# Optimization experiments

Measured on AMD Instinct MI355X. Metric: run time of the kernel, lower is better.

The kernel has to match this reference:

```python
import jax, jax.numpy as jnp
import numpy as np

IN_CH = 128
NUM_GROUPS = 32
EPS = 1e-5


def group_norm(x, weight, bias):
    b, c, h, w = x.shape
    g = NUM_GROUPS
    xg = x.reshape(b, g, c // g, h, w)
    mean = xg.mean(axis=(2, 3, 4), keepdims=True)
    var = xg.var(axis=(2, 3, 4), keepdims=True)
    xg = (xg - mean) * jax.lax.rsqrt(var + EPS)
    x = xg.reshape(b, c, h, w)
    return x * weight[None, :, None, None] + bias[None, :, None, None]


def conv1x1(x, w, b):
    # x: (b,c,h,w), w: (out,in), b: (out,)
    return jnp.einsum('oc,bchw->bohw', w, x) + b[None, :, None, None]


def setup_inputs() -> dict:
    key = jax.random.key(0)
    ks = jax.random.split(key, 6)
    b, c, h, w = 8, IN_CH, 64, 64
    scale = 1.0 / np.sqrt(c)  # xavier-ish scale for 1x1 convs
    return {
        'x': jax.random.normal(ks[0], (b, c, h, w), dtype=jnp.float32),
        'gn_weight': jnp.ones((c,), dtype=jnp.float32),
        'gn_bias': jnp.zeros((c,), dtype=jnp.float32),
        'wq': jax.random.normal(ks[1], (c, c), dtype=jnp.float32) * scale,
        'bq': jnp.zeros((c,), dtype=jnp.float32),
        'wk': jax.random.normal(ks[2], (c, c), dtype=jnp.float32) * scale,
        'bk': jnp.zeros((c,), dtype=jnp.float32),
        'wv': jax.random.normal(ks[3], (c, c), dtype=jnp.float32) * scale,
        'bv': jnp.zeros((c,), dtype=jnp.float32),
        'wo': jax.random.normal(ks[4], (c, c), dtype=jnp.float32) * scale,
        'bo': jnp.zeros((c,), dtype=jnp.float32),
        'gamma': jnp.ones((1,), dtype=jnp.float32),
    }


def reference(x, gn_weight, gn_bias, wq, bq, wk, bk, wv, bv, wo, bo, gamma):
    b, c, h, w = x.shape
    x_dash = group_norm(x, gn_weight, gn_bias)
    q = conv1x1(x_dash, wq, bq).reshape(b, c, h * w)  # (b,c,n)
    k = conv1x1(x_dash, wk, bk).reshape(b, c, h * w)
    v = conv1x1(x_dash, wv, bv).reshape(b, c, h * w)
    # attn[b,i,j] = sum_c q[b,c,i] k[b,c,j] / sqrt(c)
    attn = jnp.einsum('bci,bcj->bij', q, k) / jnp.sqrt(jnp.float32(c))
    attn = jax.nn.softmax(attn, axis=-1)
    # out[b,c,i] = sum_j v[b,c,j] attn[b,i,j]
    out = jnp.einsum('bcj,bij->bci', v, attn).reshape(b, c, h, w)
    out = conv1x1(out, wo, bo)
    return x + gamma[0] * out
```

## Files before the change

### kernel.cpp

```cpp
#include <hip/hip_runtime.h>

typedef unsigned short u16;
typedef unsigned int u32;
typedef __bf16 bf16_t;
typedef bf16_t bf16x8 __attribute__((ext_vector_type(8)));
typedef float f32x4 __attribute__((ext_vector_type(4)));
typedef u32 u32x4 __attribute__((ext_vector_type(4)));
typedef u32 u32x2 __attribute__((ext_vector_type(2)));

#define BATCH 8
#define CH 128
#define NSP 4096
#define LOG2E 1.44269504088896f

static __device__ __forceinline__ u16 f2bf(float f) {
  u32 u = __builtin_bit_cast(u32, f);
  u32 r = u + 0x7FFFu + ((u >> 16) & 1u);
  return (u16)(r >> 16);
}

static __device__ __forceinline__ bf16x8 ld_bf8(const u16* p) {
  return __builtin_bit_cast(bf16x8, *(const u32x4*)p);
}

static __device__ __forceinline__ f32x4 mfma16(bf16x8 a, bf16x8 b, f32x4 c) {
  return __builtin_amdgcn_mfma_f32_16x16x32_bf16(a, b, c, 0, 0, 0);
}

static __device__ __forceinline__ u32 cvt_pk(float lo, float hi) {
  u32 r;
  asm("v_cvt_pk_bf16_f32 %0, %1, %2" : "=v"(r) : "v"(lo), "v"(hi));
  return r;
}

static __device__ __forceinline__ float fast_exp2(float x) {
#if __has_builtin(__builtin_amdgcn_exp2f)
  return __builtin_amdgcn_exp2f(x);
#else
  return exp2f(x);
#endif
}

__global__ __launch_bounds__(256) void gn_stats_kernel(const float* __restrict__ x,
                                                       float* __restrict__ stats,
                                                       const float* __restrict__ wq,
                                                       const float* __restrict__ wk,
                                                       const float* __restrict__ wv,
                                                       const float* __restrict__ wo,
                                                       u16* __restrict__ wbf) {
  int bg = blockIdx.x;
  {
    int widx = bg * 256 + threadIdx.x;
    int m = widx >> 14, r = widx & 16383;
    const float* s = (m == 0) ? wq : (m == 1) ? wk : (m == 2) ? wv : wo;
    wbf[widx] = f2bf(s[r]);
  }
  const float4* p = (const float4*)(x + (size_t)bg * 16384);
  float s = 0.f, ss = 0.f;
  for (int i = threadIdx.x; i < 4096; i += 256) {
    float4 v = p[i];
    s += v.x + v.y + v.z + v.w;
    ss += v.x * v.x + v.y * v.y + v.z * v.z + v.w * v.w;
  }
  for (int off = 32; off; off >>= 1) {
    s += __shfl_xor(s, off);
    ss += __shfl_xor(ss, off);
  }
  __shared__ float rs[4], rss[4];
  int wave = threadIdx.x >> 6;
  if ((threadIdx.x & 63) == 0) { rs[wave] = s; rss[wave] = ss; }
  __syncthreads();
  if (threadIdx.x == 0) {
    s = rs[0] + rs[1] + rs[2] + rs[3];
    ss = rss[0] + rss[1] + rss[2] + rss[3];
    float mean = s * (1.f / 16384.f);
    float var = ss * (1.f / 16384.f) - mean * mean;
    stats[2 * bg] = mean;
    stats[2 * bg + 1] = rsqrtf(var + 1e-5f);
  }
}

__global__ __launch_bounds__(256) void qkv_kernel(const float* __restrict__ x,
                                                  const float* __restrict__ stats,
                                                  const float* __restrict__ gnw,
                                                  const float* __restrict__ gnb,
                                                  const u16* __restrict__ wqb,
                                                  const u16* __restrict__ wkb,
                                                  const u16* __restrict__ wvb,
                                                  const float* __restrict__ bq,
                                                  const float* __restrict__ bk,
                                                  const float* __restrict__ bv,
                                                  u16* __restrict__ q, u16* __restrict__ k,
                                                  u16* __restrict__ v) {
  __shared__ float tile[64][132];
  __shared__ float sc[128], sh[128];
  int b = blockIdx.y;
  int n0 = blockIdx.x * 64;
  int t = threadIdx.x;
  if (t < 128) {
    float mean = stats[2 * (b * 32 + (t >> 2))];
    float rstd = stats[2 * (b * 32 + (t >> 2)) + 1];
    float w = gnw[t];
    sc[t] = rstd * w;
    sh[t] = gnb[t] - mean * rstd * w;
  }
  __syncthreads();
  const float4* xb4 = (const float4*)(x + (size_t)b * CH * NSP);
#pragma unroll
  for (int i = 0; i < 8; ++i) {
    int idx = t + i * 256;
    int c = idx >> 4, j4 = idx & 15;
    float4 vv = xb4[(size_t)c * (NSP / 4) + (n0 >> 2) + j4];
    float s_ = sc[c], h_ = sh[c];
    tile[j4 * 4 + 0][c] = vv.x * s_ + h_;
    tile[j4 * 4 + 1][c] = vv.y * s_ + h_;
    tile[j4 * 4 + 2][c] = vv.z * s_ + h_;
    tile[j4 * 4 + 3][c] = vv.w * s_ + h_;
  }
  __syncthreads();

  int wave = t >> 6, lane = t & 63;
  int lr = lane & 15, lg = lane >> 4;
  int n_base = n0 + wave * 16;
  int row = wave * 16 + lr;

  bf16x8 xfr[4];
#pragma unroll
  for (int kk = 0; kk < 4; ++kk) {
    const float* p = &tile[row][kk * 32 + lg * 8];
    f32x4 lo = *(const f32x4*)p;
    f32x4 hi = *(const f32x4*)(p + 4);
    u32x4 xw = {cvt_pk(lo[0], lo[1]), cvt_pk(lo[2], lo[3]),
                cvt_pk(hi[0], hi[1]), cvt_pk(hi[2], hi[3])};
    xfr[kk] = __builtin_bit_cast(bf16x8, xw);
  }

  f32x4 accq[8] = {}, acck[8] = {}, accv[8] = {};
#pragma unroll
  for (int kk = 0; kk < 4; ++kk) {
    int coff = kk * 32 + lg * 8;
    bf16x8 xa = xfr[kk];
#pragma unroll
    for (int ot = 0; ot < 8; ++ot) {
      int woff = (ot * 16 + lr) * CH + coff;
      bf16x8 wqf = ld_bf8(wqb + woff);
      bf16x8 wkf = ld_bf8(wkb + woff);
      bf16x8 wvf = ld_bf8(wvb + woff);
      accq[ot] = mfma16(xa, wqf, accq[ot]);
      acck[ot] = mfma16(xa, wkf, acck[ot]);
      accv[ot] = mfma16(wvf, xa, accv[ot]);
    }
  }
  const float qscale = 0.08838834764831845f * LOG2E;
#pragma unroll
  for (int ot = 0; ot < 8; ++ot) {
    int o_col = ot * 16 + lr;
    float bqv = bq[o_col], bkv = bk[o_col];
#pragma unroll
    for (int r = 0; r < 4; ++r) {
      int nrow = n_base + lg * 4 + r;
      size_t off = ((size_t)b * NSP + nrow) * CH + o_col;
      q[off] = f2bf((accq[ot][r] + bqv) * qscale);
      k[off] = f2bf(acck[ot][r] + bkv);
    }
    int n_col = n_base + lr;
#pragma unroll
    for (int r = 0; r < 4; ++r) {
      int o_row = ot * 16 + lg * 4 + r;
      v[((size_t)b * CH + o_row) * NSP + n_col] = f2bf(accv[ot][r] + bv[o_row]);
    }
  }
}

#define KSTRIDE 136
#define VSTRIDE 72
__global__ __launch_bounds__(256, 2) void attn_kernel(const u16* __restrict__ q,
                                                      const u16* __restrict__ k,
                                                      const u16* __restrict__ v,
                                                      u16* __restrict__ part0,
                                                      u16* __restrict__ part1,
                                                      float* __restrict__ lbuf) {
  __shared__ __align__(16) u16 kbuf[2][64 * KSTRIDE];
  __shared__ __align__(16) u16 vbuf[2][128 * VSTRIDE];
  int id = blockIdx.x;
  int b = id & 7;
  int qblk = (id >> 3) & 31;
  int split = id >> 8;
  int wave = threadIdx.x >> 6, lane = threadIdx.x & 63;
  int lr = lane & 15, lg = lane >> 4;
  int i_base = qblk * 128 + wave * 32;
  int t0 = split * 32, t1 = t0 + 32;

  const u16* kg = k + (size_t)b * NSP * CH;
  const u16* vg = v + (size_t)b * CH * NSP;

  bf16x8 qa[2][4];
#pragma unroll
  for (int qt = 0; qt < 2; ++qt) {
    const u16* qrow = q + ((size_t)b * NSP + i_base + qt * 16 + lr) * CH;
#pragma unroll
    for (int kk = 0; kk < 4; ++kk) qa[qt][kk] = ld_bf8(qrow + kk * 32 + lg * 8);
  }

  int kgo[4], klo[4];
#pragma unroll
  for (int m = 0; m < 4; ++m) {
    int kr = wave * 16 + m * 4 + (lane >> 4);
    kgo[m] = kr * CH + (lane & 15) * 8;
    klo[m] = kr * KSTRIDE + (lane & 15) * 8;
  }
  int vgo[4][2], vlo[4];
  {
    int f = lane & 7;
    int p = ((lane >> 2) & 1) * 8 + (lane & 3);
#pragma unroll
    for (int w = 0; w < 4; ++w) {
      int c = wave * 32 + w * 8 + (lane >> 3);
      vgo[w][0] = c * NSP + p * 4;
      vgo[w][1] = c * NSP + (p + 4) * 4;
      vlo[w] = c * VSTRIDE + f * 8;
    }
  }

  u32x4 kstg[4];
  u32x2 vstg[4][2];
  auto KLOAD = [&](int t) {
    const u16* kt = kg + (size_t)t * (64 * CH);
#pragma unroll
    for (int m = 0; m < 4; ++m) kstg[m] = *(const u32x4*)(kt + kgo[m]);
  };
  auto VLOAD = [&](int t) {
    const u16* vt = vg + t * 64;
#pragma unroll
    for (int w = 0; w < 4; ++w) {
      vstg[w][0] = *(const u32x2*)(vt + vgo[w][0]);
      vstg[w][1] = *(const u32x2*)(vt + vgo[w][1]);
    }
  };
  auto KVWRITE = [&](int bi) {
    u16* kb2 = kbuf[bi];
    u16* vb2 = vbuf[bi];
#pragma unroll
    for (int m = 0; m < 4; ++m) *(u32x4*)(kb2 + klo[m]) = kstg[m];
#pragma unroll
    for (int w = 0; w < 4; ++w) {
      u32x4 d = {vstg[w][0][0], vstg[w][0][1], vstg[w][1][0], vstg[w][1][1]};
      *(u32x4*)(vb2 + vlo[w]) = d;
    }
  };

  KLOAD(t0);
  VLOAD(t0);
  asm volatile("s_waitcnt vmcnt(0)" ::: "memory");
  KVWRITE(0);
  KLOAD(t0 + 1);
  VLOAD(t0 + 1);
  asm volatile("s_waitcnt lgkmcnt(0)" ::: "memory");
  __builtin_amdgcn_s_barrier();
  __builtin_amdgcn_sched_barrier(0);

  f32x4 oacc[2][8] = {};
  float lsum[2] = {0.f, 0.f};

  for (int t = t0; t < t1; ++t) {
    int cur = (t - t0) & 1;
    const u16* kb = kbuf[cur];
    const u16* vb = vbuf[cur];

    f32x4 s[2][4] = {};
    __builtin_amdgcn_s_setprio(1);
#pragma unroll
    for (int kk = 0; kk < 4; ++kk) {
#pragma unroll
      for (int jt = 0; jt < 4; ++jt) {
        int row = jt * 16 + lr;
        bf16x8 kf = ld_bf8(kb + row * KSTRIDE + (kk * 4 + lg) * 8);
        s[0][jt] = mfma16(kf, qa[0][kk], s[0][jt]);
        s[1][jt] = mfma16(kf, qa[1][kk], s[1][jt]);
      }
    }
    __builtin_amdgcn_s_setprio(0);

    u32x4 paw[2][2];
#pragma unroll
    for (int qt = 0; qt < 2; ++qt) {
      float sum = 0.f;
#pragma unroll
      for (int jt = 0; jt < 4; ++jt)
#pragma unroll
        for (int r = 0; r < 4; ++r) {
          float pv = fast_exp2(s[qt][jt][r]);
          s[qt][jt][r] = pv;
          sum += pv;
        }
      lsum[qt] += sum;
#pragma unroll
      for (int kk2 = 0; kk2 < 2; ++kk2) {
        paw[qt][kk2][0] = cvt_pk(s[qt][2 * kk2][0], s[qt][2 * kk2][1]);
        paw[qt][kk2][1] = cvt_pk(s[qt][2 * kk2][2], s[qt][2 * kk2][3]);
        paw[qt][kk2][2] = cvt_pk(s[qt][2 * kk2 + 1][0], s[qt][2 * kk2 + 1][1]);
        paw[qt][kk2][3] = cvt_pk(s[qt][2 * kk2 + 1][2], s[qt][2 * kk2 + 1][3]);
      }
    }

    __builtin_amdgcn_s_setprio(1);
#pragma unroll
    for (int kk2 = 0; kk2 < 2; ++kk2) {
      bf16x8 pa0 = __builtin_bit_cast(bf16x8, paw[0][kk2]);
      bf16x8 pa1 = __builtin_bit_cast(bf16x8, paw[1][kk2]);
#pragma unroll
      for (int ct = 0; ct < 8; ++ct) {
        int c = ct * 16 + lr;
        bf16x8 vf = ld_bf8(vb + c * VSTRIDE + (kk2 * 4 + lg) * 8);
        oacc[0][ct] = mfma16(pa0, vf, oacc[0][ct]);
        oacc[1][ct] = mfma16(pa1, vf, oacc[1][ct]);
      }
    }
    __builtin_amdgcn_s_setprio(0);

    if (t + 1 < t1) {
      asm volatile("s_waitcnt vmcnt(0)" ::: "memory");
      KVWRITE(cur ^ 1);
      if (t + 2 < t1) {
        KLOAD(t + 2);
        VLOAD(t + 2);
      }
      asm volatile("s_waitcnt lgkmcnt(0)" ::: "memory");
      __builtin_amdgcn_s_barrier();
      __builtin_amdgcn_sched_barrier(0);
    }
  }

  u16* pdst = (split == 0) ? part0 : part1;
  float* ldst = lbuf + (size_t)split * (BATCH * NSP) + (size_t)b * NSP;
#pragma unroll
  for (int qt = 0; qt < 2; ++qt) {
    lsum[qt] += __shfl_xor(lsum[qt], 16);
    lsum[qt] += __shfl_xor(lsum[qt], 32);
    if (lg == 0) ldst[i_base + qt * 16 + lr] = lsum[qt];
#pragma unroll
    for (int r = 0; r < 4; ++r) {
      int i = i_base + qt * 16 + lg * 4 + r;
      u16* row = pdst + ((size_t)b * NSP + i) * CH;
#pragma unroll
      for (int ct = 0; ct < 8; ++ct) row[ct * 16 + lr] = f2bf(oacc[qt][ct][r]);
    }
  }
}

__global__ __launch_bounds__(256) void proj_kernel(const u16* __restrict__ p0,
                                                   const u16* __restrict__ p1,
                                                   const float* __restrict__ lbuf,
                                                   const u16* __restrict__ wob,
                                                   const float* __restrict__ bo,
                                                   const float* __restrict__ gamma,
                                                   const float* __restrict__ x,
                                                   float* __restrict__ out) {
  int b = blockIdx.y;
  int wave = threadIdx.x >> 6, lane = threadIdx.x & 63;
  int lr = lane & 15, lg = lane >> 4;
  int n_base = blockIdx.x * 64 + wave * 16;
  int nrow = n_base + lr;
  float linv = 1.f / (lbuf[(size_t)b * NSP + nrow] +
                      lbuf[(size_t)BATCH * NSP + (size_t)b * NSP + nrow]);
  const u16* r0 = p0 + ((size_t)b * NSP + nrow) * CH;
  const u16* r1 = p1 + ((size_t)b * NSP + nrow) * CH;
  f32x4 acc[8] = {};
#pragma unroll
  for (int kk = 0; kk < 4; ++kk) {
    int coff = kk * 32 + lg * 8;
    bf16x8 a = ld_bf8(r0 + coff);
    bf16x8 bb = ld_bf8(r1 + coff);
    u32 w0 = cvt_pk(((float)a[0] + (float)bb[0]) * linv, ((float)a[1] + (float)bb[1]) * linv);
    u32 w1 = cvt_pk(((float)a[2] + (float)bb[2]) * linv, ((float)a[3] + (float)bb[3]) * linv);
    u32 w2 = cvt_pk(((float)a[4] + (float)bb[4]) * linv, ((float)a[5] + (float)bb[5]) * linv);
    u32 w3 = cvt_pk(((float)a[6] + (float)bb[6]) * linv, ((float)a[7] + (float)bb[7]) * linv);
    u32x4 wv = {w0, w1, w2, w3};
    bf16x8 ofrag = __builtin_bit_cast(bf16x8, wv);
#pragma unroll
    for (int ot = 0; ot < 8; ++ot) {
      bf16x8 wf = ld_bf8(wob + (ot * 16 + lr) * CH + coff);
      acc[ot] = mfma16(wf, ofrag, acc[ot]);
    }
  }
  float g = gamma[0];
  int n_col = n_base + lr;
#pragma unroll
  for (int ot = 0; ot < 8; ++ot) {
#pragma unroll
    for (int r = 0; r < 4; ++r) {
      int o_row = ot * 16 + lg * 4 + r;
      size_t off = ((size_t)b * CH + o_row) * NSP + n_col;
      out[off] = x[off] + g * (acc[ot][r] + bo[o_row]);
    }
  }
}

extern "C" void kernel_launch(void* const* d_in, const int* in_sizes, int n_in,
                              void* d_out, int out_size, void* d_ws, size_t ws_size,
                              hipStream_t stream) {
  const float* x = (const float*)d_in[0];
  const float* gnw = (const float*)d_in[1];
  const float* gnb = (const float*)d_in[2];
  const float* wq = (const float*)d_in[3];
  const float* bq = (const float*)d_in[4];
  const float* wk = (const float*)d_in[5];
  const float* bk = (const float*)d_in[6];
  const float* wv = (const float*)d_in[7];
  const float* bv = (const float*)d_in[8];
  const float* wo = (const float*)d_in[9];
  const float* bo = (const float*)d_in[10];
  const float* gamma = (const float*)d_in[11];
  float* out = (float*)d_out;

  const size_t BUF = (size_t)BATCH * NSP * CH * sizeof(u16);
  char* ws = (char*)d_ws;
  u16* wbf = (u16*)ws;
  float* stats = (float*)(ws + 131072);
  u16* xd = (u16*)(ws + 262144);
  u16* qb = (u16*)(ws + 262144 + BUF);
  u16* kb = (u16*)(ws + 262144 + 2 * BUF);
  u16* vb = (u16*)(ws + 262144 + 3 * BUF);
  float* lbuf = (float*)(ws + 262144 + 4 * BUF);
  const size_t need = 262144 + 4 * BUF + 262144;
  if (ws_size < need) return;
  u16* part1 = (ws_size >= need + BUF) ? (u16*)(ws + need) : qb;

  gn_stats_kernel<<<256, 256, 0, stream>>>(x, stats, wq, wk, wv, wo, wbf);
  qkv_kernel<<<dim3(64, 8), 256, 0, stream>>>(x, stats, gnw, gnb, wbf, wbf + 16384,
                                              wbf + 32768, bq, bk, bv, qb, kb, vb);
  attn_kernel<<<512, 256, 0, stream>>>(qb, kb, vb, xd, part1, lbuf);
  proj_kernel<<<dim3(64, 8), 256, 0, stream>>>(xd, part1, lbuf, wbf + 49152, bo, gamma,
                                               x, out);
}
```

Baseline: 135.3 us.

## Stage K/V via direct global-to-LDS loads with swizzled layout and 3-way split

Replaces register-staged K/V tile copies in the attention kernel with global_load_lds direct transfers, using an XOR-swizzled layout written by the QKV kernel instead of padded LDS strides. V becomes single-buffered to cut LDS use, which allows 3 blocks per CU, and the key range is split three ways across 768 blocks. A separate combine kernel normalises the three partials before projection, reusing the output and K buffers as scratch. This trades an extra kernel launch and more partial-buffer traffic for better occupancy and less LDS staging overhead.

Result: slower. 141.7 us (+4.8%).

```diff
diff --git a/kernel.cpp b/kernel.cpp
--- a/kernel.cpp
+++ b/kernel.cpp
@@ -6,7 +6,6 @@
 typedef bf16_t bf16x8 __attribute__((ext_vector_type(8)));
 typedef float f32x4 __attribute__((ext_vector_type(4)));
 typedef u32 u32x4 __attribute__((ext_vector_type(4)));
-typedef u32 u32x2 __attribute__((ext_vector_type(2)));
 
 #define BATCH 8
 #define CH 128
@@ -39,6 +38,11 @@
 #else
   return exp2f(x);
 #endif
+}
+
+static __device__ __forceinline__ void gl2lds16(const u16* g, u16* l) {
+  __builtin_amdgcn_global_load_lds((const __attribute__((address_space(1))) void*)g,
+                                   (__attribute__((address_space(3))) void*)l, 16, 0, 0);
 }
 
 __global__ __launch_bounds__(256) void gn_stats_kernel(const float* __restrict__ x,
@@ -152,6 +156,9 @@
     }
   }
   const float qscale = 0.08838834764831845f * LOG2E;
+  int jj = wave * 16 + lr;
+  int frv = (jj >> 5) * 4 + ((jj & 15) >> 2);
+  int ev = (lr & 3) + ((wave & 1) << 2);
 #pragma unroll
   for (int ot = 0; ot < 8; ++ot) {
     int o_col = ot * 16 + lr;
@@ -159,29 +166,29 @@
 #pragma unroll
     for (int r = 0; r < 4; ++r) {
       int nrow = n_base + lg * 4 + r;
-      size_t off = ((size_t)b * NSP + nrow) * CH + o_col;
-      q[off] = f2bf((accq[ot][r] + bqv) * qscale);
-      k[off] = f2bf(acck[ot][r] + bkv);
-    }
-    int n_col = n_base + lr;
+      q[((size_t)b * NSP + nrow) * CH + o_col] = f2bf((accq[ot][r] + bqv) * qscale);
+      int cperm = ((((o_col >> 3) ^ (nrow & 7)) << 3)) | (o_col & 7);
+      k[((size_t)b * NSP + nrow) * CH + cperm] = f2bf(acck[ot][r] + bkv);
+    }
 #pragma unroll
     for (int r = 0; r < 4; ++r) {
-      int o_row = ot * 16 + lg * 4 + r;
-      v[((size_t)b * CH + o_row) * NSP + n_col] = f2bf(accv[ot][r] + bv[o_row]);
-    }
-  }
-}
-
-#define KSTRIDE 136
-#define VSTRIDE 72
-__global__ __launch_bounds__(256, 2) void attn_kernel(const u16* __restrict__ q,
+      int c = ot * 16 + lg * 4 + r;
+      int slot = frv ^ (c & 7);
+      v[((size_t)(b * CH + c)) * NSP + blockIdx.x * 64 + slot * 8 + ev] =
+          f2bf(accv[ot][r] + bv[c]);
+    }
+  }
+}
+
+__global__ __launch_bounds__(256, 3) void attn_kernel(const u16* __restrict__ q,
                                                       const u16* __restrict__ k,
                                                       const u16* __restrict__ v,
                                                       u16* __restrict__ part0,
                                                       u16* __restrict__ part1,
+                                                      u16* __restrict__ part2,
                                                       float* __restrict__ lbuf) {
-  __shared__ __align__(16) u16 kbuf[2][64 * KSTRIDE];
-  __shared__ __align__(16) u16 vbuf[2][128 * VSTRIDE];
+  __shared__ __align__(16) u16 kbuf[2][64 * 128];
+  __shared__ __align__(16) u16 vbuf[128 * 64];
   int id = blockIdx.x;
   int b = id & 7;
   int qblk = (id >> 3) & 31;
@@ -189,7 +196,8 @@
   int wave = threadIdx.x >> 6, lane = threadIdx.x & 63;
   int lr = lane & 15, lg = lane >> 4;
   int i_base = qblk * 128 + wave * 32;
-  int t0 = split * 32, t1 = t0 + 32;
+  int t0 = (split * 64) / 3;
+  int t1 = ((split + 1) * 64) / 3;
 
   const u16* kg = k + (size_t)b * NSP * CH;
   const u16* vg = v + (size_t)b * CH * NSP;
@@ -201,63 +209,24 @@
 #pragma unroll
     for (int kk = 0; kk < 4; ++kk) qa[qt][kk] = ld_bf8(qrow + kk * 32 + lg * 8);
   }
-
-  int kgo[4], klo[4];
-#pragma unroll
-  for (int m = 0; m < 4; ++m) {
-    int kr = wave * 16 + m * 4 + (lane >> 4);
-    kgo[m] = kr * CH + (lane & 15) * 8;
-    klo[m] = kr * KSTRIDE + (lane & 15) * 8;
-  }
-  int vgo[4][2], vlo[4];
-  {
-    int f = lane & 7;
-    int p = ((lane >> 2) & 1) * 8 + (lane & 3);
-#pragma unroll
-    for (int w = 0; w < 4; ++w) {
-      int c = wave * 32 + w * 8 + (lane >> 3);
-      vgo[w][0] = c * NSP + p * 4;
-      vgo[w][1] = c * NSP + (p + 4) * 4;
-      vlo[w] = c * VSTRIDE + f * 8;
-    }
-  }
-
-  u32x4 kstg[4];
-  u32x2 vstg[4][2];
-  auto KLOAD = [&](int t) {
-    const u16* kt = kg + (size_t)t * (64 * CH);
-#pragma unroll
-    for (int m = 0; m < 4; ++m) kstg[m] = *(const u32x4*)(kt + kgo[m]);
+  asm volatile("s_waitcnt vmcnt(0)" ::: "memory");
+
+  auto STAGEK = [&](int t, int bi) {
+    const u16* src = kg + ((size_t)(t * 64 + wave * 16)) * CH + lane * 8;
+    u16* dst = &kbuf[bi][wave * 16 * 128];
+#pragma unroll
+    for (int g = 0; g < 4; ++g) gl2lds16(src + g * 512, dst + g * 512);
   };
-  auto VLOAD = [&](int t) {
-    const u16* vt = vg + t * 64;
-#pragma unroll
-    for (int w = 0; w < 4; ++w) {
-      vstg[w][0] = *(const u32x2*)(vt + vgo[w][0]);
-      vstg[w][1] = *(const u32x2*)(vt + vgo[w][1]);
-    }
+  int vco = wave * 32 + (lane >> 3);
+  auto STAGEV = [&](int t) {
+    const u16* src = vg + t * 64 + (lane & 7) * 8;
+    u16* dst = &vbuf[wave * 32 * 64];
+#pragma unroll
+    for (int g = 0; g < 4; ++g) gl2lds16(src + (size_t)(vco + g * 8) * NSP, dst + g * 512);
   };
-  auto KVWRITE = [&](int bi) {
-    u16* kb2 = kbuf[bi];
-    u16* vb2 = vbuf[bi];
-#pragma unroll
-    for (int m = 0; m < 4; ++m) *(u32x4*)(kb2 + klo[m]) = kstg[m];
-#pragma unroll
-    for (int w = 0; w < 4; ++w) {
-      u32x4 d = {vstg[w][0][0], vstg[w][0][1], vstg[w][1][0], vstg[w][1][1]};
-      *(u32x4*)(vb2 + vlo[w]) = d;
-    }
-  };
-
-  KLOAD(t0);
-  VLOAD(t0);
-  asm volatile("s_waitcnt vmcnt(0)" ::: "memory");
-  KVWRITE(0);
-  KLOAD(t0 + 1);
-  VLOAD(t0 + 1);
-  asm volatile("s_waitcnt lgkmcnt(0)" ::: "memory");
-  __builtin_amdgcn_s_barrier();
-  __builtin_amdgcn_sched_barrier(0);
+
+  STAGEK(t0, 0);
+  STAGEV(t0);
 
   f32x4 oacc[2][8] = {};
   float lsum[2] = {0.f, 0.f};
@@ -265,7 +234,14 @@
   for (int t = t0; t < t1; ++t) {
     int cur = (t - t0) & 1;
     const u16* kb = kbuf[cur];
-    const u16* vb = vbuf[cur];
+    if (t + 1 < t1) {
+      STAGEK(t + 1, cur ^ 1);
+      asm volatile("s_waitcnt vmcnt(4)" ::: "memory");
+    } else {
+      asm volatile("s_waitcnt vmcnt(0)" ::: "memory");
+    }
+    __builtin_amdgcn_s_barrier();
+    __builtin_amdgcn_sched_barrier(0);
 
     f32x4 s[2][4] = {};
     __builtin_amdgcn_s_setprio(1);
@@ -274,7 +250,7 @@
 #pragma unroll
       for (int jt = 0; jt < 4; ++jt) {
         int row = jt * 16 + lr;
-        bf16x8 kf = ld_bf8(kb + row * KSTRIDE + (kk * 4 + lg) * 8);
+        bf16x8 kf = ld_bf8(kb + row * 128 + ((((kk << 2) + lg) ^ (row & 7)) << 3));
         s[0][jt] = mfma16(kf, qa[0][kk], s[0][jt]);
         s[1][jt] = mfma16(kf, qa[1][kk], s[1][jt]);
       }
@@ -311,27 +287,18 @@
 #pragma unroll
       for (int ct = 0; ct < 8; ++ct) {
         int c = ct * 16 + lr;
-        bf16x8 vf = ld_bf8(vb + c * VSTRIDE + (kk2 * 4 + lg) * 8);
+        bf16x8 vf = ld_bf8(vbuf + c * 64 + ((((kk2 << 2) + lg) ^ (c & 7)) << 3));
         oacc[0][ct] = mfma16(pa0, vf, oacc[0][ct]);
         oacc[1][ct] = mfma16(pa1, vf, oacc[1][ct]);
       }
     }
     __builtin_amdgcn_s_setprio(0);
 
-    if (t + 1 < t1) {
-      asm volatile("s_waitcnt vmcnt(0)" ::: "memory");
-      KVWRITE(cur ^ 1);
-      if (t + 2 < t1) {
-        KLOAD(t + 2);
-        VLOAD(t + 2);
-      }
-      asm volatile("s_waitcnt lgkmcnt(0)" ::: "memory");
-      __builtin_amdgcn_s_barrier();
-      __builtin_amdgcn_sched_barrier(0);
-    }
-  }
-
-  u16* pdst = (split == 0) ? part0 : part1;
+    __builtin_amdgcn_s_barrier();
+    if (t + 1 < t1) STAGEV(t + 1);
+  }
+
+  u16* pdst = (split == 0) ? part0 : (split == 1) ? part1 : part2;
   float* ldst = lbuf + (size_t)split * (BATCH * NSP) + (size_t)b * NSP;
 #pragma unroll
   for (int qt = 0; qt < 2; ++qt) {
@@ -348,9 +315,27 @@
   }
 }
 
-__global__ __launch_bounds__(256) void proj_kernel(const u16* __restrict__ p0,
-                                                   const u16* __restrict__ p1,
-                                                   const float* __restrict__ lbuf,
+__global__ __launch_bounds__(256) void combine_kernel(const u16* __restrict__ p0,
+                                                      const u16* __restrict__ p1,
+                                                      const u16* __restrict__ p2,
+                                                      const float* __restrict__ lbuf,
+                                                      u16* __restrict__ omid) {
+  int idx = blockIdx.x * 256 + threadIdx.x;
+  int row = idx >> 4, coff = (idx & 15) * 8;
+  const int BN = BATCH * NSP;
+  float l = lbuf[row] + lbuf[BN + row] + lbuf[2 * BN + row];
+  float inv = 1.f / l;
+  bf16x8 a = ld_bf8(p0 + (size_t)row * CH + coff);
+  bf16x8 bb = ld_bf8(p1 + (size_t)row * CH + coff);
+  bf16x8 cc = ld_bf8(p2 + (size_t)row * CH + coff);
+  u16 outv[8];
+#pragma unroll
+  for (int e = 0; e < 8; ++e)
+    outv[e] = f2bf(((float)a[e] + (float)bb[e] + (float)cc[e]) * inv);
+  *(u32x4*)(omid + (size_t)row * CH + coff) = *(const u32x4*)outv;
+}
+
+__global__ __launch_bounds__(256) void proj_kernel(const u16* __restrict__ omid,
                                                    const u16* __restrict__ wob,
                                                    const float* __restrict__ bo,
                                                    const float* __restrict__ gamma,
@@ -360,23 +345,12 @@
   int wave = threadIdx.x >> 6, lane = threadIdx.x & 63;
   int lr = lane & 15, lg = lane >> 4;
   int n_base = blockIdx.x * 64 + wave * 16;
-  int nrow = n_base + lr;
-  float linv = 1.f / (lbuf[(size_t)b * NSP + nrow] +
-                      lbuf[(size_t)BATCH * NSP + (size_t)b * NSP + nrow]);
-  const u16* r0 = p0 + ((size_t)b * NSP + nrow) * CH;
-  const u16* r1 = p1 + ((size_t)b * NSP + nrow) * CH;
+  const u16* orow = omid + ((size_t)b * NSP + n_base + lr) * CH;
   f32x4 acc[8] = {};
 #pragma unroll
   for (int kk = 0; kk < 4; ++kk) {
     int coff = kk * 32 + lg * 8;
-    bf16x8 a = ld_bf8(r0 + coff);
-    bf16x8 bb = ld_bf8(r1 + coff);
-    u32 w0 = cvt_pk(((float)a[0] + (float)bb[0]) * linv, ((float)a[1] + (float)bb[1]) * linv);
-    u32 w1 = cvt_pk(((float)a[2] + (float)bb[2]) * linv, ((float)a[3] + (float)bb[3]) * linv);
-    u32 w2 = cvt_pk(((float)a[4] + (float)bb[4]) * linv, ((float)a[5] + (float)bb[5]) * linv);
-    u32 w3 = cvt_pk(((float)a[6] + (float)bb[6]) * linv, ((float)a[7] + (float)bb[7]) * linv);
-    u32x4 wv = {w0, w1, w2, w3};
-    bf16x8 ofrag = __builtin_bit_cast(bf16x8, wv);
+    bf16x8 ofrag = ld_bf8(orow + coff);
 #pragma unroll
     for (int ot = 0; ot < 8; ++ot) {
       bf16x8 wf = ld_bf8(wob + (ot * 16 + lr) * CH + coff);
@@ -422,14 +396,15 @@
   u16* kb = (u16*)(ws + 262144 + 2 * BUF);
   u16* vb = (u16*)(ws + 262144 + 3 * BUF);
   float* lbuf = (float*)(ws + 262144 + 4 * BUF);
-  const size_t need = 262144 + 4 * BUF + 262144;
+  const size_t need = 262144 + 4 * BUF + 393216;
   if (ws_size < need) return;
   u16* part1 = (ws_size >= need + BUF) ? (u16*)(ws + need) : qb;
+  u16* part2 = (u16*)d_out;
 
   gn_stats_kernel<<<256, 256, 0, stream>>>(x, stats, wq, wk, wv, wo, wbf);
   qkv_kernel<<<dim3(64, 8), 256, 0, stream>>>(x, stats, gnw, gnb, wbf, wbf + 16384,
                                               wbf + 32768, bq, bk, bv, qb, kb, vb);
-  attn_kernel<<<512, 256, 0, stream>>>(qb, kb, vb, xd, part1, lbuf);
-  proj_kernel<<<dim3(64, 8), 256, 0, stream>>>(xd, part1, lbuf, wbf + 49152, bo, gamma,
-                                               x, out);
-}
+  attn_kernel<<<768, 256, 0, stream>>>(qb, kb, vb, xd, part1, part2, lbuf);
+  combine_kernel<<<2048, 256, 0, stream>>>(xd, part1, part2, lbuf, kb);
+  proj_kernel<<<dim3(64, 8), 256, 0, stream>>>(kb, wbf + 49152, bo, gamma, x, out);
+}
```
